# Performance work log

Hardware: AMD Instinct MI355X
Metric: run time of the kernel (lower is better)

The kernel has to match this reference:

```python
import jax, jax.numpy as jnp
import numpy as np

MASK_FILL = -100.0


def setup_inputs() -> dict:
    key = jax.random.key(0)
    k1, k2, k3, k4 = jax.random.split(key, 4)
    B, S1, S2, D_IN, D_OUT = 8, 2048, 2048, 1024, 1024
    input1 = jax.random.normal(k1, (B, S1, D_IN), dtype=jnp.float32)
    input2 = jax.random.normal(k2, (B, S2, D_OUT), dtype=jnp.float32)
    input_mask = jax.random.randint(k3, (B, S1), 0, 2) > 0  # bool [B,S1]
    # kaiming_uniform-ish init scale for weight [out_features, in_features]
    bound = 1.0 / np.sqrt(D_IN)
    weight = jax.random.uniform(k4, (D_OUT, D_IN), dtype=jnp.float32,
                                minval=-bound, maxval=bound)
    return {"input1": input1, "input2": input2,
            "input_mask": input_mask, "weight": weight}


def reference(input1, input2, input_mask, weight):
    # out1 = F.linear(input1, weight): [B,S1,in] @ [in,out] -> [B,S1,out]
    out1 = jnp.einsum('bsd,od->bso', input1, weight)
    # scores: [B,S1,out] x [B,S2,out]^T -> [B,S1,S2]
    scores = jnp.einsum('bso,bto->bst', out1, input2)
    # out2[~input_mask] = -100 : mask is [B,S1], zeroes whole rows of scores
    scores = jnp.where(input_mask[:, :, None], scores, MASK_FILL)
    # softmax over S1 (dim=1), then attn^T @ input1 -> [B,S2,in]
    attn = jax.nn.softmax(scores, axis=1)
    satt = jnp.einsum('bst,bsd->btd', attn, input1)
    return satt
```

## Files before the change

kernel.cpp:

```cpp
#include <hip/hip_runtime.h>


typedef short s16x8 __attribute__((ext_vector_type(8)));
typedef float f32x4 __attribute__((ext_vector_type(4)));
typedef unsigned short u16;
typedef unsigned short u16x8 __attribute__((ext_vector_type(8)));
typedef _Float16 f16x8v __attribute__((ext_vector_type(8)));

#define B_ 8
#define S1_ 2048
#define S2_ 2048
#define D_ 1024

__device__ __forceinline__ float b2f(u16 u) {
  return __uint_as_float(((unsigned int)u) << 16);
}
__device__ __forceinline__ u16 f2b(float f) {
  unsigned int x = __float_as_uint(f);
  return (u16)((x + 0x7FFFu + ((x >> 16) & 1u)) >> 16);
}
__device__ __forceinline__ u16 f2h(float f) {
  _Float16 h = (_Float16)f;
  return __builtin_bit_cast(u16, h);
}
__device__ __forceinline__ float h2f(u16 u) {
  return (float)__builtin_bit_cast(_Float16, u);
}
__device__ __forceinline__ void gload16(const void* g, void* l) {
  __builtin_amdgcn_global_load_lds(
      (const __attribute__((address_space(1))) unsigned int*)g,
      (__attribute__((address_space(3))) unsigned int*)l, 16, 0, 0);
}

template <bool F16>
__device__ __forceinline__ f32x4 mfma16(s16x8 a, s16x8 b, f32x4 c) {
  if constexpr (F16)
    return __builtin_amdgcn_mfma_f32_16x16x32_f16(
        __builtin_bit_cast(f16x8v, a), __builtin_bit_cast(f16x8v, b), c, 0, 0,
        0);
  else
    return __builtin_amdgcn_mfma_f32_16x16x32_bf16(a, b, c, 0, 0, 0);
}


__global__ __launch_bounds__(256) void split_h_kernel(
    const float* __restrict__ in, u16* __restrict__ h, int n4) {
  int i = blockIdx.x * 256 + threadIdx.x;
  if (i >= n4) return;
  f32x4 v = ((const f32x4*)in)[i];
  ushort4 o;
  o.x = f2h(v[0]);
  o.y = f2h(v[1]);
  o.z = f2h(v[2]);
  o.w = f2h(v[3]);
  ((ushort4*)h)[i] = o;
}

__global__ __launch_bounds__(256) void zero_kernel(float* __restrict__ p,
                                                   int n) {
  int i = blockIdx.x * 256 + threadIdx.x;
  if (i < n) p[i] = 0.f;
}

__global__ __launch_bounds__(256) void compact_kernel(
    const int* __restrict__ mask, int* __restrict__ sidx,
    int* __restrict__ cnt, int* __restrict__ kr) {
  const int b = blockIdx.x;
  const int* mb = mask + (long)b * S1_;
  int* sb = sidx + (long)b * S1_;
  const int t = threadIdx.x;
  const int lane = t & 63, w = t >> 6;
  __shared__ int wsum[4];
  int loc[8], c = 0;
#pragma unroll
  for (int j = 0; j < 8; ++j) {
    loc[j] = (mb[t * 8 + j] != 0);
    c += loc[j];
  }
  int inc = c;
  for (int off = 1; off < 64; off <<= 1) {
    int v = __shfl_up(inc, off, 64);
    if (lane >= off) inc += v;
  }
  if (lane == 63) wsum[w] = inc;
  __syncthreads();
  int woff = 0;
#pragma unroll
  for (int i = 0; i < 4; ++i)
    if (i < w) woff += wsum[i];
  int pos = woff + inc - c;
#pragma unroll
  for (int j = 0; j < 8; ++j)
    if (loc[j]) sb[pos++] = t * 8 + j;
  if (t == 255) {
    int tot = woff + inc;
    cnt[b] = tot;
    int r = (tot + 127) & ~127;
    if (r < 256) r = 256;
    kr[b] = r;
  }
}

template <int NSEG, int MODE, bool F16, bool INDA, bool DYNK>
__global__ __launch_bounds__(512, 2) void gemm8(
    const u16* __restrict__ A0, const u16* __restrict__ A1,
    const u16* __restrict__ A2, const u16* __restrict__ B0,
    const u16* __restrict__ B1, const u16* __restrict__ B2,
    void* __restrict__ Cp, u16* __restrict__ C2, int K, int lda, int ldb,
    int ldc, long sA, long sB, long sC, const int* __restrict__ sidx,
    int sidxStride, const int* __restrict__ cntArr,
    const int* __restrict__ krArr, float* __restrict__ lvec, int lvecStride) {
  __shared__ __align__(16) u16 Abuf0[8192];
  __shared__ __align__(16) u16 Abuf1[8192];
  __shared__ __align__(16) u16 Abuf2[8192];
  __shared__ __align__(16) u16 Abuf3[8192];
  __shared__ __align__(16) u16 Bbuf0[8192];
  __shared__ __align__(16) u16 Bbuf1[8192];
  __shared__ __align__(16) u16 Bbuf2[8192];
  __shared__ __align__(16) u16 Bbuf3[8192];

  const int gx = gridDim.x, gy = gridDim.y;
  int flat = blockIdx.x + gx * (blockIdx.y + gy * blockIdx.z);
  const int total = gx * gy * (int)gridDim.z;
  const int cpx = total >> 3;
  flat = (flat & 7) * cpx + (flat >> 3);
  const int bx = flat % gx;
  const int rem0 = flat / gx;
  const int by = rem0 % gy;
  const int bz = rem0 / gy;

  if constexpr (INDA) {
    if (by * 256 >= krArr[bz]) return;
  }
  if constexpr (MODE == 1) {
    if (bx * 256 >= krArr[bz]) return;
  }

  const int tid = threadIdx.x;
  const int lane = tid & 63;
  const int wid = tid >> 6;
  const int wr = wid >> 2;
  const int wn = wid & 3;

  const int Keff = DYNK ? krArr[bz] : K;
  const int tps = Keff >> 5;
  const int NT = NSEG * tps;

  const int srow = tid >> 2;
  const int kch = (tid & 3) ^ ((srow >> 1) & 3);
  int ar0g = by * 256 + srow, ar1g = ar0g + 128;
  if constexpr (INDA) {
    const int* sx = sidx + (long)bz * sidxStride;
    ar0g = sx[ar0g];
    ar1g = sx[ar1g];
  }
  const long aRow1 = (long)ar0g * lda + kch * 8;
  const long aRow2 = (long)ar1g * lda + kch * 8;
  const long bRow1 = (long)(bx * 256 + srow) * ldb + kch * 8;
  const long bRow2 = (long)(bx * 256 + srow + 128) * ldb + kch * 8;

  const u16* aBase0 = A0 + (long)bz * sA;
  const u16* bBase0 = B0 + (long)bz * sB;
  const u16* aBase1 = (NSEG > 1) ? A1 + (long)bz * sA : aBase0;
  const u16* bBase1 = (NSEG > 1) ? B1 + (long)bz * sB : bBase0;
  const u16* aBase2 = (NSEG > 2) ? A2 + (long)bz * sA : aBase0;
  const u16* bBase2 = (NSEG > 2) ? B2 + (long)bz * sB : bBase0;

  const int lr = lane & 15;
  const int kg = lane >> 4;
  const int arow0 = wr * 128 + lr;
  const int aOffU = arow0 * 32 + (kg ^ ((arow0 >> 1) & 3)) * 8;
  const int brow0 = wn * 64 + lr;
  const int bOffU = brow0 * 32 + (kg ^ ((brow0 >> 1) & 3)) * 8;

  const f32x4 z4 = {0.f, 0.f, 0.f, 0.f};
  f32x4 acc[8][4];
#pragma unroll
  for (int i = 0; i < 8; ++i)
#pragma unroll
    for (int j = 0; j < 4; ++j) acc[i][j] = z4;

  int s_rem = 0, s_seg = 0;
  const u16* aS = aBase0;
  const u16* bS = bBase0;

#define STAGE_AB(DA_, DB_)                                                   \
  {                                                                          \
    gload16(aS + aRow1 + s_rem * 32, &DA_[wid * 512]);                       \
    gload16(aS + aRow2 + s_rem * 32, &DA_[wid * 512 + 4096]);                \
    gload16(bS + bRow1 + s_rem * 32, &DB_[wid * 512]);                       \
    gload16(bS + bRow2 + s_rem * 32, &DB_[wid * 512 + 4096]);                \
    if (++s_rem == tps) {                                                    \
      s_rem = 0;                                                             \
      ++s_seg;                                                               \
      aS = (s_seg == 1) ? aBase1 : aBase2;                                   \
      bS = (s_seg == 1) ? bBase1 : bBase2;                                   \
    }                                                                        \
  }

  STAGE_AB(Abuf0, Bbuf0);
  STAGE_AB(Abuf1, Bbuf1);
  STAGE_AB(Abuf2, Bbuf2);
  asm volatile("s_waitcnt vmcnt(8)" ::: "memory");
  __builtin_amdgcn_s_barrier();

#define ITER(AS_, BS_, DA_, DB_, VM_, STG_)                                  \
  {                                                                          \
    s16x8 a0[4], a1[4], bfr[4];                                              \
    _Pragma("unroll") for (int m_ = 0; m_ < 4; ++m_) a0[m_] =                \
        *(const s16x8*)&AS_[aOffU + m_ * 512];                               \
    _Pragma("unroll") for (int n_ = 0; n_ < 4; ++n_) bfr[n_] =               \
        *(const s16x8*)&BS_[bOffU + n_ * 512];                               \
    _Pragma("unroll") for (int m_ = 0; m_ < 4; ++m_) a1[m_] =                \
        *(const s16x8*)&AS_[aOffU + (m_ + 4) * 512];                         \
    if (STG_) {                                                              \
      gload16(aS + aRow1 + s_rem * 32, &DA_[wid * 512]);                     \
      gload16(aS + aRow2 + s_rem * 32, &DA_[wid * 512 + 4096]);              \
    }                                                                        \
    asm volatile("" ::: "memory");                                           \
    __builtin_amdgcn_s_barrier();                                            \
    __builtin_amdgcn_sched_barrier(0);                                       \
    __builtin_amdgcn_s_setprio(1);                                           \
    _Pragma("unroll") for (int m_ = 0; m_ < 4; ++m_)                         \
        _Pragma("unroll") for (int n_ = 0; n_ < 4; ++n_) acc[m_][n_] =       \
            mfma16<F16>(a0[m_], bfr[n_], acc[m_][n_]);                       \
    __builtin_amdgcn_s_setprio(0);                                           \
    if (STG_) {                                                              \
      gload16(bS + bRow1 + s_rem * 32, &DB_[wid * 512]);                     \
      gload16(bS + bRow2 + s_rem * 32, &DB_[wid * 512 + 4096]);              \
      if (++s_rem == tps) {                                                  \
        s_rem = 0;                                                           \
        ++s_seg;                                                             \
        aS = (s_seg == 1) ? aBase1 : aBase2;                                 \
        bS = (s_seg == 1) ? bBase1 : bBase2;                                 \
      }                                                                      \
    }                                                                        \
    asm volatile("s_waitcnt " VM_ ::: "memory");                             \
    __builtin_amdgcn_s_barrier();                                            \
    __builtin_amdgcn_sched_barrier(0);                                       \
    __builtin_amdgcn_s_setprio(1);                                           \
    _Pragma("unroll") for (int m_ = 0; m_ < 4; ++m_)                         \
        _Pragma("unroll") for (int n_ = 0; n_ < 4; ++n_) acc[m_ + 4][n_] =   \
            mfma16<F16>(a1[m_], bfr[n_], acc[m_ + 4][n_]);                   \
    __builtin_amdgcn_s_setprio(0);                                           \
  }

  for (int t = 0; t < NT - 4; t += 4) {
    ITER(Abuf0, Bbuf0, Abuf3, Bbuf3, "vmcnt(8)", true);
    ITER(Abuf1, Bbuf1, Abuf0, Bbuf0, "vmcnt(8)", true);
    ITER(Abuf2, Bbuf2, Abuf1, Bbuf1, "vmcnt(8)", true);
    ITER(Abuf3, Bbuf3, Abuf2, Bbuf2, "vmcnt(8)", true);
  }
  ITER(Abuf0, Bbuf0, Abuf3, Bbuf3, "vmcnt(8)", true);
  ITER(Abuf1, Bbuf1, Abuf0, Bbuf0, "vmcnt(4)", false);
  ITER(Abuf2, Bbuf2, Abuf1, Bbuf1, "vmcnt(0)", false);
  ITER(Abuf3, Bbuf3, Abuf2, Bbuf2, "vmcnt(0)", false);

#undef ITER
#undef STAGE_AB

  const int row0 = by * 256 + wr * 128 + kg * 4;
  const int col0 = bx * 256 + wn * 64 + lr;

  if (MODE == 0) {
    u16* Ch = (u16*)Cp + (long)bz * sC;
    u16* Cl = C2 + (long)bz * sC;
#pragma unroll
    for (int m = 0; m < 8; ++m)
#pragma unroll
      for (int n = 0; n < 4; ++n)
#pragma unroll
        for (int r = 0; r < 4; ++r) {
          float v = acc[m][n][r];
          long idx = (long)(row0 + m * 16 + r) * ldc + (col0 + n * 16);
          if (F16) {
            u16 h = f2h(v);
            Ch[idx] = h;
            Cl[idx] = f2h(v - h2f(h));
          } else {
            u16 h = f2b(v);
            Ch[idx] = h;
            Cl[idx] = f2b(v - b2f(h));
          }
        }
  } else if (MODE == 1) {
    u16* Cb = (u16*)Cp + (long)bz * sC;
    float* lvout = lvec + (long)bz * lvecStride;
    const int cn = cntArr[bz];
    int mcol[4];
#pragma unroll
    for (int n = 0; n < 4; ++n) mcol[n] = (col0 + n * 16) < cn;
#pragma unroll
    for (int m = 0; m < 8; ++m)
#pragma unroll
      for (int r = 0; r < 4; ++r) {
        float rv = 0.f;
#pragma unroll
        for (int n = 0; n < 4; ++n) {
          float v = acc[m][n][r];
          v = mcol[n] ? __expf(v - 100.0f) : 0.0f;
          Cb[(long)(row0 + m * 16 + r) * ldc + (col0 + n * 16)] = f2b(v);
          rv += v;
        }
        rv += __shfl_xor(rv, 1, 16);
        rv += __shfl_xor(rv, 2, 16);
        rv += __shfl_xor(rv, 4, 16);
        rv += __shfl_xor(rv, 8, 16);
        if (lr == 0) atomicAdd(&lvout[row0 + m * 16 + r], rv);
      }
  } else {
    float* Cb = (float*)Cp + (long)bz * sC;
    const float* lb = lvec + (long)bz * lvecStride;
#pragma unroll
    for (int m = 0; m < 8; ++m) {
      float sc[4];
#pragma unroll
      for (int r = 0; r < 4; ++r) {
        float dv = lb[row0 + m * 16 + r];
        sc[r] = (dv > 0.0f) ? 1.0f / dv : 0.0f;
      }
#pragma unroll
      for (int n = 0; n < 4; ++n)
#pragma unroll
        for (int r = 0; r < 4; ++r)
          Cb[(long)(row0 + m * 16 + r) * ldc + (col0 + n * 16)] =
              acc[m][n][r] * sc[r];
    }
  }
}


__device__ __forceinline__ void split8(const float* __restrict__ g, s16x8& h,
                                       s16x8& l) {
  f32x4 a = *(const f32x4*)g;
  f32x4 b = *(const f32x4*)(g + 4);
#pragma unroll
  for (int j = 0; j < 8; ++j) {
    float x = (j < 4) ? a[j] : b[j - 4];
    u16 hu = f2b(x);
    h[j] = (short)hu;
    l[j] = (short)f2b(x - b2f(hu));
  }
}

template <int MODE>
__global__ __launch_bounds__(256, 2) void gemm_k(
    const void* __restrict__ Ap, const void* __restrict__ Bp,
    const u16* __restrict__ Blo, void* __restrict__ Cp, u16* __restrict__ C2,
    int K, int ldc, long sA, long sB, long sC, const int* __restrict__ mask,
    int maskStride, const float* __restrict__ lvec, int lvecStride) {
  constexpr bool TRI = (MODE != 2);
  __shared__ s16x8 AsH[512];
  __shared__ s16x8 BsH[512];
  __shared__ s16x8 AsL[TRI ? 512 : 1];
  __shared__ s16x8 BsL[TRI ? 512 : 1];

  const int z = blockIdx.z;
  const int tid = threadIdx.x;
  const int lane = tid & 63;
  const int wid = tid >> 6;

  const f32x4 z4 = {0.f, 0.f, 0.f, 0.f};
  f32x4 acc[4][4];
#pragma unroll
  for (int i = 0; i < 4; ++i)
#pragma unroll
    for (int j = 0; j < 4; ++j) acc[i][j] = z4;

  const int wm = (wid & 1) * 64;
  const int wn = (wid >> 1) * 64;
  const int lrow = lane & 15;
  const int kofs = (lane >> 4) * 8;
  const int srow = tid >> 1;
  const int shalf = (tid & 1) * 16;
  const int lidx = (srow * 32 + shalf) >> 3;

  const u16* AsHu = (const u16*)AsH;
  const u16* BsHu = (const u16*)BsH;
  const u16* AsLu = (const u16*)AsL;
  const u16* BsLu = (const u16*)BsL;

  for (int k0 = 0; k0 < K; k0 += 32) {
    if (MODE == 2) {
      const u16* Ab = (const u16*)Ap + z * sA + (long)blockIdx.y * 128 * K;
      const u16* Bb = (const u16*)Bp + z * sB + (long)blockIdx.x * 128 * K;
      const u16* ga = Ab + (long)srow * K + k0 + shalf;
      const u16* gb = Bb + (long)srow * K + k0 + shalf;
      AsH[lidx] = *(const s16x8*)ga;
      AsH[lidx + 1] = *(const s16x8*)(ga + 8);
      BsH[lidx] = *(const s16x8*)gb;
      BsH[lidx + 1] = *(const s16x8*)(gb + 8);
    } else {
      const float* Ab = (const float*)Ap + z * sA + (long)blockIdx.y * 128 * K;
      const float* ga = Ab + (long)srow * K + k0 + shalf;
      split8(ga, AsH[lidx], AsL[lidx]);
      split8(ga + 8, AsH[lidx + 1], AsL[lidx + 1]);
      if (MODE == 0) {
        const float* Bb = (const float*)Bp + z * sB + (long)blockIdx.x * 128 * K;
        const float* gb = Bb + (long)srow * K + k0 + shalf;
        split8(gb, BsH[lidx], BsL[lidx]);
        split8(gb + 8, BsH[lidx + 1], BsL[lidx + 1]);
      } else {
        const u16* Bh = (const u16*)Bp + z * sB + (long)blockIdx.x * 128 * K;
        const u16* Bl = Blo + z * sB + (long)blockIdx.x * 128 * K;
        const u16* gh = Bh + (long)srow * K + k0 + shalf;
        const u16* gl = Bl + (long)srow * K + k0 + shalf;
        BsH[lidx] = *(const s16x8*)gh;
        BsH[lidx + 1] = *(const s16x8*)(gh + 8);
        BsL[lidx] = *(const s16x8*)gl;
        BsL[lidx + 1] = *(const s16x8*)(gl + 8);
      }
    }
    __syncthreads();
    s16x8 ah[4], bh[4], al[4], bl[4];
#pragma unroll
    for (int t = 0; t < 4; ++t) {
      ah[t] = *(const s16x8*)&AsHu[(wm + t * 16 + lrow) * 32 + kofs];
      bh[t] = *(const s16x8*)&BsHu[(wn + t * 16 + lrow) * 32 + kofs];
      if (TRI) {
        al[t] = *(const s16x8*)&AsLu[(wm + t * 16 + lrow) * 32 + kofs];
        bl[t] = *(const s16x8*)&BsLu[(wn + t * 16 + lrow) * 32 + kofs];
      }
    }
#pragma unroll
    for (int i = 0; i < 4; ++i)
#pragma unroll
      for (int j = 0; j < 4; ++j) {
        acc[i][j] = __builtin_amdgcn_mfma_f32_16x16x32_bf16(ah[i], bh[j],
                                                            acc[i][j], 0, 0, 0);
        if (TRI) {
          acc[i][j] = __builtin_amdgcn_mfma_f32_16x16x32_bf16(
              al[i], bh[j], acc[i][j], 0, 0, 0);
          acc[i][j] = __builtin_amdgcn_mfma_f32_16x16x32_bf16(
              ah[i], bl[j], acc[i][j], 0, 0, 0);
        }
      }
    __syncthreads();
  }

  const int row0 = blockIdx.y * 128 + wm + (lane >> 4) * 4;
  const int col0 = blockIdx.x * 128 + wn + lrow;

  if (MODE == 0) {
    u16* Ch = (u16*)Cp;
#pragma unroll
    for (int i = 0; i < 4; ++i)
#pragma unroll
      for (int j = 0; j < 4; ++j)
#pragma unroll
        for (int r = 0; r < 4; ++r) {
          float v = acc[i][j][r];
          long idx = (long)(row0 + i * 16 + r) * ldc + (col0 + j * 16);
          u16 h = f2b(v);
          Ch[idx] = h;
          C2[idx] = f2b(v - b2f(h));
        }
  } else if (MODE == 1) {
    u16* Cb = (u16*)Cp + z * sC;
    const int* mb = mask + (long)z * maskStride;
    int mcol[4];
#pragma unroll
    for (int j = 0; j < 4; ++j) mcol[j] = mb[col0 + j * 16];
#pragma unroll
    for (int i = 0; i < 4; ++i)
#pragma unroll
      for (int j = 0; j < 4; ++j)
#pragma unroll
        for (int r = 0; r < 4; ++r) {
          float v = acc[i][j][r];
          v = mcol[j] ? __expf(v - 100.0f) : 0.0f;
          Cb[(long)(row0 + i * 16 + r) * ldc + (col0 + j * 16)] = f2b(v);
        }
  } else {
    float* Cb = (float*)Cp + z * sC;
    const float* lb = lvec + (long)z * lvecStride;
    float scale[4][4];
#pragma unroll
    for (int i = 0; i < 4; ++i)
#pragma unroll
      for (int r = 0; r < 4; ++r) {
        float dv = lb[row0 + i * 16 + r];
        scale[i][r] = (dv > 0.0f) ? 1.0f / dv : 0.0f;
      }
#pragma unroll
    for (int i = 0; i < 4; ++i)
#pragma unroll
      for (int j = 0; j < 4; ++j)
#pragma unroll
        for (int r = 0; r < 4; ++r)
          Cb[(long)(row0 + i * 16 + r) * ldc + (col0 + j * 16)] =
              acc[i][j][r] * scale[i][r];
  }
}


__global__ __launch_bounds__(256) void rowsum_kernel(const u16* __restrict__ E,
                                                     float* __restrict__ l) {
  const int row = blockIdx.x * 4 + (threadIdx.x >> 6);
  const int lane = threadIdx.x & 63;
  const u16* p = E + (size_t)row * S1_;
  float s = 0.f;
#pragma unroll
  for (int j = 0; j < 4; ++j) {
    u16x8 v = *(const u16x8*)(p + (j * 64 + lane) * 8);
#pragma unroll
    for (int k = 0; k < 8; ++k) s += b2f(v[k]);
  }
#pragma unroll
  for (int off = 32; off; off >>= 1) s += __shfl_down(s, off, 64);
  if (lane == 0) l[row] = s;
}

__global__ __launch_bounds__(256) void transposeC_kernel(
    const float* __restrict__ in, const int* __restrict__ sidx,
    const int* __restrict__ cnt, const int* __restrict__ kr,
    u16* __restrict__ out) {
  __shared__ u16 tile[64][66];
  const int b = blockIdx.z;
  const int s0 = blockIdx.x * 64;
  if (s0 >= kr[b]) return;
  const int cn = cnt[b];
  const int* sx = sidx + (long)b * S1_;
  const float* ib = in + (size_t)b * S1_ * D_;
  u16* ob = out + (size_t)b * D_ * S1_;
  const int d0 = blockIdx.y * 64;
  const int t = threadIdx.x;
  const int tr = t >> 4;
  const int tc = (t & 15) * 4;
#pragma unroll
  for (int i = 0; i < 4; ++i) {
    int row = tr + i * 16;
    int j = s0 + row;
    if (j < cn) {
      f32x4 v = *(const f32x4*)(ib + (size_t)sx[j] * D_ + d0 + tc);
      tile[row][tc + 0] = f2b(v[0]);
      tile[row][tc + 1] = f2b(v[1]);
      tile[row][tc + 2] = f2b(v[2]);
      tile[row][tc + 3] = f2b(v[3]);
    } else {
      tile[row][tc + 0] = 0;
      tile[row][tc + 1] = 0;
      tile[row][tc + 2] = 0;
      tile[row][tc + 3] = 0;
    }
  }
  __syncthreads();
#pragma unroll
  for (int i = 0; i < 4; ++i) {
    int drow = tr + i * 16;
    ushort4 w;
    w.x = tile[tc + 0][drow];
    w.y = tile[tc + 1][drow];
    w.z = tile[tc + 2][drow];
    w.w = tile[tc + 3][drow];
    *(ushort4*)(ob + (size_t)(d0 + drow) * S1_ + s0 + tc) = w;
  }
}

__global__ __launch_bounds__(256) void transpose_kernel(
    const float* __restrict__ in, u16* __restrict__ out) {
  __shared__ u16 tile[64][66];
  const int b = blockIdx.z;
  const float* ib = in + (size_t)b * S1_ * D_;
  u16* ob = out + (size_t)b * D_ * S1_;
  const int s0 = blockIdx.x * 64;
  const int d0 = blockIdx.y * 64;
  const int t = threadIdx.x;
  const int tr = t >> 4;
  const int tc = (t & 15) * 4;
#pragma unroll
  for (int i = 0; i < 4; ++i) {
    int row = tr + i * 16;
    f32x4 v = *(const f32x4*)(ib + (size_t)(s0 + row) * D_ + d0 + tc);
    tile[row][tc + 0] = f2b(v[0]);
    tile[row][tc + 1] = f2b(v[1]);
    tile[row][tc + 2] = f2b(v[2]);
    tile[row][tc + 3] = f2b(v[3]);
  }
  __syncthreads();
#pragma unroll
  for (int i = 0; i < 4; ++i) {
    int drow = tr + i * 16;
    ushort4 w;
    w.x = tile[tc + 0][drow];
    w.y = tile[tc + 1][drow];
    w.z = tile[tc + 2][drow];
    w.w = tile[tc + 3][drow];
    *(ushort4*)(ob + (size_t)(d0 + drow) * S1_ + s0 + tc) = w;
  }
}


extern "C" void kernel_launch(void* const* d_in, const int* in_sizes, int n_in,
                              void* d_out, int out_size, void* d_ws,
                              size_t ws_size, hipStream_t stream) {
  const float* in1 = (const float*)d_in[0];
  const float* in2 = (const float*)d_in[1];
  const int* mask = (const int*)d_in[2];
  const float* W = (const float*)d_in[3];
  float* out = (float*)d_out;
  char* ws = (char*)d_ws;
  const size_t MB = 1024 * 1024;
  const size_t KB = 1024;
  dim3 blk(256);
  dim3 blk512(512);

  const size_t FULL_WS = 196 * MB + 64 * 1024;
  if (ws_size >= FULL_WS) {
    u16* in1_h = (u16*)(ws + 0);
    u16* in2_h = (u16*)(ws + 32 * MB);
    u16* W_h = (u16*)(ws + 64 * MB);
    u16* ET = (u16*)(ws + 66 * MB);
    u16* out1C_h = (u16*)(ws + 130 * MB);
    u16* out1C_l = (u16*)(ws + 162 * MB);
    float* lv = (float*)(ws + 194 * MB);
    int* sidx = (int*)(ws + 194 * MB + 64 * KB);
    int* cnt = (int*)(ws + 194 * MB + 128 * KB);
    int* kr = cnt + 8;
    u16* in1TC = (u16*)(ws + 0);

    split_h_kernel<<<dim3(16384), blk, 0, stream>>>(in1, in1_h,
                                                    B_ * S1_ * D_ / 4);
    split_h_kernel<<<dim3(16384), blk, 0, stream>>>(in2, in2_h,
                                                    B_ * S2_ * D_ / 4);
    split_h_kernel<<<dim3(1024), blk, 0, stream>>>(W, W_h, D_ * D_ / 4);
    zero_kernel<<<dim3(128), blk, 0, stream>>>(lv, 32768);
    compact_kernel<<<dim3(B_), blk, 0, stream>>>(mask, sidx, cnt, kr);

    gemm8<1, 0, true, true, false><<<dim3(4, 8, B_), blk512, 0, stream>>>(
        in1_h, in1_h, in1_h, W_h, W_h, W_h, out1C_h, out1C_l, D_, D_, D_, D_,
        (long)S1_ * D_, 0L, (long)S1_ * D_, sidx, S1_, cnt, kr, nullptr, 0);

    transposeC_kernel<<<dim3(S1_ / 64, D_ / 64, B_), blk, 0, stream>>>(
        in1, sidx, cnt, kr, in1TC);

    gemm8<2, 1, true, false, false><<<dim3(8, 8, B_), blk512, 0, stream>>>(
        in2_h, in2_h, in2_h, out1C_h, out1C_l, out1C_l, ET, nullptr, D_, D_,
        D_, S1_, (long)S2_ * D_, (long)S1_ * D_, (long)S2_ * S1_, nullptr, 0,
        cnt, kr, lv, S2_);

    gemm8<1, 2, false, false, true><<<dim3(4, 8, B_), blk512, 0, stream>>>(
        ET, ET, ET, in1TC, in1TC, in1TC, out, nullptr, 0, S1_, S1_, D_,
        (long)S2_ * S1_, (long)D_ * S1_, (long)S2_ * D_, nullptr, 0, cnt, kr,
        lv, S2_);
  } else {
    u16* out1_hi = (u16*)ws;
    u16* out1_lo = (u16*)(ws + 32 * MB);
    u16* ET = (u16*)(ws + 64 * MB);
    float* lv = (float*)(ws + 128 * MB);
    u16* in1T = out1_hi;

    gemm_k<0><<<dim3(8, 128, 1), blk, 0, stream>>>(
        in1, W, nullptr, out1_hi, out1_lo, D_, D_, 0, 0, 0, nullptr, 0,
        nullptr, 0);
    gemm_k<1><<<dim3(16, 16, B_), blk, 0, stream>>>(
        in2, out1_hi, out1_lo, ET, nullptr, D_, S1_, (long)S2_ * D_,
        (long)S1_ * D_, (long)S2_ * S1_, mask, S1_, nullptr, 0);
    rowsum_kernel<<<dim3(B_ * S2_ / 4), blk, 0, stream>>>(ET, lv);
    transpose_kernel<<<dim3(S1_ / 64, D_ / 64, B_), blk, 0, stream>>>(in1, in1T);
    gemm_k<2><<<dim3(8, 16, B_), blk, 0, stream>>>(
        ET, in1T, nullptr, out, nullptr, S1_, D_, (long)S2_ * S1_,
        (long)D_ * S1_, (long)S2_ * D_, nullptr, 0, lv, S2_);
  }
}
```

Measured before the change: 390.4 us.

## Gather masked in1 rows into compact buffer and pad ET leading dimension

Replaces the full-size f16 conversion of input1 with a gather kernel that converts only the compacted (unmasked) rows, so the first GEMM reads contiguous rows instead of indexing through sidx. It also pads the leading dimension of ET and the transposed input1 to 2064 to avoid power-of-two stride conflicts, and reorders the transpose to run after the score GEMM. This reduces conversion traffic and removes the indexed loads, at the cost of a larger workspace layout whose new offsets must still fit within the size check.

```diff
diff --git a/kernel.cpp b/kernel.cpp
--- a/kernel.cpp
+++ b/kernel.cpp
@@ -11,6 +11,7 @@
 #define S1_ 2048
 #define S2_ 2048
 #define D_ 1024
+#define LDET 2064
 
 __device__ __forceinline__ float b2f(u16 u) {
   return __uint_as_float(((unsigned int)u) << 16);
@@ -101,14 +102,37 @@
   }
 }
 
-template <int NSEG, int MODE, bool F16, bool INDA, bool DYNK>
+__global__ __launch_bounds__(256) void gather_split_kernel(
+    const float* __restrict__ in, const int* __restrict__ sidx,
+    const int* __restrict__ cnt, const int* __restrict__ kr,
+    u16* __restrict__ outh) {
+  const int b = blockIdx.y;
+  const int r = blockIdx.x;
+  if (r >= kr[b]) return;
+  u16* orow = outh + ((size_t)b * S1_ + r) * D_;
+  const int t = threadIdx.x;
+  if (r < cnt[b]) {
+    const int src = sidx[(size_t)b * S1_ + r];
+    f32x4 v = *(const f32x4*)(in + ((size_t)b * S1_ + src) * D_ + t * 4);
+    ushort4 o;
+    o.x = f2h(v[0]);
+    o.y = f2h(v[1]);
+    o.z = f2h(v[2]);
+    o.w = f2h(v[3]);
+    *(ushort4*)(orow + t * 4) = o;
+  } else {
+    ushort4 z = {0, 0, 0, 0};
+    *(ushort4*)(orow + t * 4) = z;
+  }
+}
+
+template <int NSEG, int MODE, bool F16, bool EXITM, bool DYNK>
 __global__ __launch_bounds__(512, 2) void gemm8(
     const u16* __restrict__ A0, const u16* __restrict__ A1,
     const u16* __restrict__ A2, const u16* __restrict__ B0,
     const u16* __restrict__ B1, const u16* __restrict__ B2,
     void* __restrict__ Cp, u16* __restrict__ C2, int K, int lda, int ldb,
-    int ldc, long sA, long sB, long sC, const int* __restrict__ sidx,
-    int sidxStride, const int* __restrict__ cntArr,
+    int ldc, long sA, long sB, long sC, const int* __restrict__ cntArr,
     const int* __restrict__ krArr, float* __restrict__ lvec, int lvecStride) {
   __shared__ __align__(16) u16 Abuf0[8192];
   __shared__ __align__(16) u16 Abuf1[8192];
@@ -129,7 +153,7 @@
   const int by = rem0 % gy;
   const int bz = rem0 / gy;
 
-  if constexpr (INDA) {
+  if constexpr (EXITM) {
     if (by * 256 >= krArr[bz]) return;
   }
   if constexpr (MODE == 1) {
@@ -148,14 +172,8 @@
 
   const int srow = tid >> 2;
   const int kch = (tid & 3) ^ ((srow >> 1) & 3);
-  int ar0g = by * 256 + srow, ar1g = ar0g + 128;
-  if constexpr (INDA) {
-    const int* sx = sidx + (long)bz * sidxStride;
-    ar0g = sx[ar0g];
-    ar1g = sx[ar1g];
-  }
-  const long aRow1 = (long)ar0g * lda + kch * 8;
-  const long aRow2 = (long)ar1g * lda + kch * 8;
+  const long aRow1 = (long)(by * 256 + srow) * lda + kch * 8;
+  const long aRow2 = (long)(by * 256 + srow + 128) * lda + kch * 8;
   const long bRow1 = (long)(bx * 256 + srow) * ldb + kch * 8;
   const long bRow2 = (long)(bx * 256 + srow + 128) * ldb + kch * 8;
 
@@ -522,7 +540,7 @@
   const int cn = cnt[b];
   const int* sx = sidx + (long)b * S1_;
   const float* ib = in + (size_t)b * S1_ * D_;
-  u16* ob = out + (size_t)b * D_ * S1_;
+  u16* ob = out + (size_t)b * D_ * LDET;
   const int d0 = blockIdx.y * 64;
   const int t = threadIdx.x;
   const int tr = t >> 4;
@@ -553,7 +571,7 @@
     w.y = tile[tc + 1][drow];
     w.z = tile[tc + 2][drow];
     w.w = tile[tc + 3][drow];
-    *(ushort4*)(ob + (size_t)(d0 + drow) * S1_ + s0 + tc) = w;
+    *(ushort4*)(ob + (size_t)(d0 + drow) * LDET + s0 + tc) = w;
   }
 }
 
@@ -601,48 +619,46 @@
   float* out = (float*)d_out;
   char* ws = (char*)d_ws;
   const size_t MB = 1024 * 1024;
-  const size_t KB = 1024;
   dim3 blk(256);
   dim3 blk512(512);
 
   const size_t FULL_WS = 196 * MB + 64 * 1024;
   if (ws_size >= FULL_WS) {
-    u16* in1_h = (u16*)(ws + 0);
-    u16* in2_h = (u16*)(ws + 32 * MB);
-    u16* W_h = (u16*)(ws + 64 * MB);
-    u16* ET = (u16*)(ws + 66 * MB);
-    u16* out1C_h = (u16*)(ws + 130 * MB);
-    u16* out1C_l = (u16*)(ws + 162 * MB);
-    float* lv = (float*)(ws + 194 * MB);
-    int* sidx = (int*)(ws + 194 * MB + 64 * KB);
-    int* cnt = (int*)(ws + 194 * MB + 128 * KB);
+    u16* in1C_h = (u16*)(ws + 0);
+    u16* in1TC = (u16*)(ws + 0);
+    u16* in2_h = (u16*)(ws + 33816576UL);
+    u16* W_h = (u16*)(ws + 67371008UL);
+    u16* ET = (u16*)(ws + 69468160UL);
+    u16* out1C_h = (u16*)(ws + 137101312UL);
+    u16* out1C_l = (u16*)(ws + 170655744UL);
+    float* lv = (float*)(ws + 204210176UL);
+    int* sidx = (int*)(ws + 204275712UL);
+    int* cnt = (int*)(ws + 204341248UL);
     int* kr = cnt + 8;
-    u16* in1TC = (u16*)(ws + 0);
-
-    split_h_kernel<<<dim3(16384), blk, 0, stream>>>(in1, in1_h,
-                                                    B_ * S1_ * D_ / 4);
+
     split_h_kernel<<<dim3(16384), blk, 0, stream>>>(in2, in2_h,
                                                     B_ * S2_ * D_ / 4);
     split_h_kernel<<<dim3(1024), blk, 0, stream>>>(W, W_h, D_ * D_ / 4);
     zero_kernel<<<dim3(128), blk, 0, stream>>>(lv, 32768);
     compact_kernel<<<dim3(B_), blk, 0, stream>>>(mask, sidx, cnt, kr);
+    gather_split_kernel<<<dim3(S1_, B_), blk, 0, stream>>>(in1, sidx, cnt, kr,
+                                                           in1C_h);
 
     gemm8<1, 0, true, true, false><<<dim3(4, 8, B_), blk512, 0, stream>>>(
-        in1_h, in1_h, in1_h, W_h, W_h, W_h, out1C_h, out1C_l, D_, D_, D_, D_,
-        (long)S1_ * D_, 0L, (long)S1_ * D_, sidx, S1_, cnt, kr, nullptr, 0);
+        in1C_h, in1C_h, in1C_h, W_h, W_h, W_h, out1C_h, out1C_l, D_, D_, D_,
+        D_, (long)S1_ * D_, 0L, (long)S1_ * D_, cnt, kr, nullptr, 0);
+
+    gemm8<2, 1, true, false, false><<<dim3(8, 8, B_), blk512, 0, stream>>>(
+        in2_h, in2_h, in2_h, out1C_h, out1C_l, out1C_l, ET, nullptr, D_, D_,
+        D_, LDET, (long)S2_ * D_, (long)S1_ * D_, (long)S1_ * LDET, cnt, kr,
+        lv, S2_);
 
     transposeC_kernel<<<dim3(S1_ / 64, D_ / 64, B_), blk, 0, stream>>>(
         in1, sidx, cnt, kr, in1TC);
 
-    gemm8<2, 1, true, false, false><<<dim3(8, 8, B_), blk512, 0, stream>>>(
-        in2_h, in2_h, in2_h, out1C_h, out1C_l, out1C_l, ET, nullptr, D_, D_,
-        D_, S1_, (long)S2_ * D_, (long)S1_ * D_, (long)S2_ * S1_, nullptr, 0,
-        cnt, kr, lv, S2_);
-
     gemm8<1, 2, false, false, true><<<dim3(4, 8, B_), blk512, 0, stream>>>(
-        ET, ET, ET, in1TC, in1TC, in1TC, out, nullptr, 0, S1_, S1_, D_,
-        (long)S2_ * S1_, (long)D_ * S1_, (long)S2_ * D_, nullptr, 0, cnt, kr,
-        lv, S2_);
+        ET, ET, ET, in1TC, in1TC, in1TC, out, nullptr, 0, LDET, LDET, D_,
+        (long)S1_ * LDET, (long)D_ * LDET, (long)S2_ * D_, cnt, kr, lv, S2_);
   } else {
     u16* out1_hi = (u16*)ws;
     u16* out1_lo = (u16*)(ws + 32 * MB);
```

Result: no change. 392.7 us (+0.6%).
